# Optimization experiments

Hardware: AMD Instinct MI355X
Metric: run time of the kernel (lower is better)

The kernel has to match this reference:

```python
import jax, jax.numpy as jnp
import numpy as np

N = 50000      # nodes
E = 800000     # edges
IN = 128       # in_channels
HID = 64       # hidden_channels (per head)
HEADS = 2      # GAT heads
OUT = 64       # out_channels (classes)


def segment_softmax(e, seg, num_segments):
    # softmax of per-edge scores grouped by destination node
    m = jax.ops.segment_max(e, seg, num_segments=num_segments)
    ex = jnp.exp(e - m[seg])
    s = jax.ops.segment_sum(ex, seg, num_segments=num_segments)
    return ex / s[seg]


def setup_inputs() -> dict:
    key = jax.random.key(0)
    ks = jax.random.split(key, 12)
    sc = 0.05
    return {
        "x": jax.random.normal(ks[0], (N, IN), dtype=jnp.float32),
        "edge_index": jax.random.randint(ks[1], (2, E), 0, N),
        # GATConv params: lin (no bias), att_src/att_dst, output bias
        "W1": jax.random.normal(ks[2], (IN, HEADS * HID), dtype=jnp.float32) * sc,
        "att_src": jax.random.normal(ks[3], (HEADS, HID), dtype=jnp.float32) * sc,
        "att_dst": jax.random.normal(ks[4], (HEADS, HID), dtype=jnp.float32) * sc,
        "b1": jnp.zeros((HEADS * HID,), dtype=jnp.float32),
        # TransformerConv params (heads=1): q/k/v linears + skip linear
        "Wq": jax.random.normal(ks[5], (HEADS * HID, OUT), dtype=jnp.float32) * sc,
        "bq": jnp.zeros((OUT,), dtype=jnp.float32),
        "Wk": jax.random.normal(ks[6], (HEADS * HID, OUT), dtype=jnp.float32) * sc,
        "bk": jnp.zeros((OUT,), dtype=jnp.float32),
        "Wv": jax.random.normal(ks[7], (HEADS * HID, OUT), dtype=jnp.float32) * sc,
        "bv": jnp.zeros((OUT,), dtype=jnp.float32),
        "Wskip": jax.random.normal(ks[8], (HEADS * HID, OUT), dtype=jnp.float32) * sc,
        "bskip": jnp.zeros((OUT,), dtype=jnp.float32),
    }


def reference(x, edge_index, W1, att_src, att_dst, b1,
              Wq, bq, Wk, bk, Wv, bv, Wskip, bskip):
    n = x.shape[0]
    # ---- GATConv (concat=True, add_self_loops=True, negative_slope=0.2) ----
    loops = jnp.arange(n)
    src = jnp.concatenate([edge_index[0], loops])  # message source j
    dst = jnp.concatenate([edge_index[1], loops])  # message target i
    h = (x @ W1).reshape(n, HEADS, HID)            # [N,H,C]
    a_src = (h * att_src).sum(-1)                  # [N,H]
    a_dst = (h * att_dst).sum(-1)                  # [N,H]
    e = jax.nn.leaky_relu(a_src[src] + a_dst[dst], 0.2)   # [E+N,H]
    alpha = segment_softmax(e, dst, n)                     # [E+N,H]
    out1 = jax.ops.segment_sum(alpha[..., None] * h[src], dst, num_segments=n)
    x1 = jax.nn.relu(out1.reshape(n, HEADS * HID) + b1)    # [N,H*C]
    # ---- TransformerConv (heads=1, root_weight=True, no self-loops) ----
    q = x1 @ Wq + bq
    k = x1 @ Wk + bk
    v = x1 @ Wv + bv
    s2, d2 = edge_index[0], edge_index[1]
    scores = (q[d2] * k[s2]).sum(-1) / jnp.sqrt(jnp.float32(OUT))  # [E]
    al = segment_softmax(scores, d2, n)
    agg = jax.ops.segment_sum(al[:, None] * v[s2], d2, num_segments=n)
    out = agg + x1 @ Wskip + bskip
    return jax.nn.log_softmax(out, axis=1)
```

## Files before the change

### kernel.cpp

```cpp
#include <hip/hip_runtime.h>
#include <math.h>

typedef unsigned short u16;
typedef unsigned int u32;
typedef unsigned char u8;

using bf16x8 = __attribute__((ext_vector_type(8))) short;
using f32x4  = __attribute__((ext_vector_type(4))) float;
typedef __attribute__((ext_vector_type(2))) float vf2;

__device__ __forceinline__ float lrelu02(float x){ return x > 0.f ? x : 0.2f * x; }

__device__ __forceinline__ float bf2f(u16 u){
  union { u32 i; float f; } v; v.i = ((u32)u) << 16; return v.f;
}
__device__ __forceinline__ u16 f2bf(float f){
  union { float ff; u32 i; } v; v.ff = f;
  u32 x = v.i;
  return (u16)((x + 0x7fffu + ((x >> 16) & 1u)) >> 16);
}
__device__ __forceinline__ u32 pack2(float lo, float hi){
  return (u32)f2bf(lo) | ((u32)f2bf(hi) << 16);
}
__device__ __forceinline__ u8 f2fp8(float v){
  return (u8)(__builtin_amdgcn_cvt_pk_fp8_f32(v, v, 0, false) & 0xff);
}
__device__ __forceinline__ vf2 fma2(vf2 a, vf2 b, vf2 c){
  return __builtin_elementwise_fma(a, b, c);
}

__global__ __launch_bounds__(256) void prep_w_kernel(const float* __restrict__ W1,
                                                     const float* __restrict__ Wq,
                                                     const float* __restrict__ Wk,
                                                     const float* __restrict__ Wv,
                                                     const float* __restrict__ Ws,
                                                     const float* __restrict__ att_src,
                                                     const float* __restrict__ att_dst,
                                                     u16* __restrict__ w1t,
                                                     u16* __restrict__ wt2,
                                                     u16* __restrict__ wxt){
  int idx = blockIdx.x * 256 + threadIdx.x;
  if (idx < 16384){
    int j = idx >> 7, k = idx & 127;
    w1t[j * 128 + k] = f2bf(W1[k * 128 + j]);
  } else if (idx < 49152){
    int i = idx - 16384;
    int mat = i >> 13;
    int r = i & 8191;
    int j = r >> 7, k = r & 127;
    const float* W = (mat == 0) ? Wq : (mat == 1) ? Wk : (mat == 2) ? Wv : Ws;
    wt2[(mat * 64 + j) * 128 + k] = f2bf(W[k * 64 + j]);
  } else if (idx < 49664){
    int i = idx - 49152;
    int j = i >> 7, k = i & 127;
    const float* av = (j & 2) ? att_dst : att_src;
    int head = j & 1;
    float s = 0.f;
#pragma unroll 8
    for (int c = 0; c < 64; c++) s += W1[k * 128 + head * 64 + c] * av[head * 64 + c];
    wxt[j * 128 + k] = f2bf(s);
  } else if (idx < 51200){
    int i = idx - 49664;
    wxt[512 + i] = 0;
  }
}

__global__ __launch_bounds__(256) void gemm1_mfma(const float* __restrict__ x,
                                                  const u16* __restrict__ w1t,
                                                  const u16* __restrict__ wxt,
                                                  u8* __restrict__ h8,
                                                  float* __restrict__ asrc,
                                                  float* __restrict__ adst, int n){
  __shared__ u8 lds8[64 * 128];
  int wid = threadIdx.x >> 6, lane = threadIdx.x & 63;
  int rl = lane & 15, kh = lane >> 4;
  int br = blockIdx.x * 64 + wid * 16;
  int arow = br + rl; if (arow > n - 1) arow = n - 1;
  const float* ab = x + (size_t)arow * 128 + kh * 8;
  f32x4 acc[9];
#pragma unroll
  for (int t = 0; t < 9; t++) acc[t] = (f32x4){0.f, 0.f, 0.f, 0.f};
#pragma unroll
  for (int ks = 0; ks < 4; ks++){
    float4 xa = *(const float4*)(ab + ks * 32);
    float4 xb = *(const float4*)(ab + ks * 32 + 4);
    union { bf16x8 v; u32 w[4]; } au;
    au.w[0] = pack2(xa.x, xa.y);
    au.w[1] = pack2(xa.z, xa.w);
    au.w[2] = pack2(xb.x, xb.y);
    au.w[3] = pack2(xb.z, xb.w);
    bf16x8 a = au.v;
#pragma unroll
    for (int t = 0; t < 8; t++){
      bf16x8 b = *(const bf16x8*)(w1t + (size_t)(t * 16 + rl) * 128 + ks * 32 + kh * 8);
      acc[t] = __builtin_amdgcn_mfma_f32_16x16x32_bf16(a, b, acc[t], 0, 0, 0);
    }
    bf16x8 bx = *(const bf16x8*)(wxt + (size_t)rl * 128 + ks * 32 + kh * 8);
    acc[8] = __builtin_amdgcn_mfma_f32_16x16x32_bf16(a, bx, acc[8], 0, 0, 0);
  }
#pragma unroll
  for (int r = 0; r < 4; r++){
    int rloc = wid * 16 + kh * 4 + r;
#pragma unroll
    for (int t = 0; t < 8; t++)
      lds8[rloc * 128 + t * 16 + rl] = f2fp8(acc[t][r]);
    int orow = br + kh * 4 + r;
    if (orow < n && rl < 4){
      float vlv = acc[8][r];
      if (rl < 2) asrc[orow * 2 + rl] = vlv;
      else        adst[orow * 2 + (rl - 2)] = vlv;
    }
  }
  int rrow = wid * 16 + (lane >> 2);
  int cb = (lane & 3) * 32;
  int grow = blockIdx.x * 64 + rrow;
  if (grow < n){
    uint4 v0 = *(const uint4*)&lds8[rrow * 128 + cb];
    uint4 v1 = *(const uint4*)&lds8[rrow * 128 + cb + 16];
    uint4* gp = (uint4*)(h8 + (size_t)grow * 128 + cb);
    gp[0] = v0;
    gp[1] = v1;
  }
}

__global__ __launch_bounds__(256) void gemm2_mfma(const u16* __restrict__ x1bf,
                                                  const u16* __restrict__ wt2,
                                                  const float* __restrict__ bq,
                                                  const float* __restrict__ bk,
                                                  const float* __restrict__ bv,
                                                  const float* __restrict__ bs,
                                                  float* __restrict__ q,
                                                  u8* __restrict__ kv8,
                                                  float* __restrict__ skip, int n){
  int wid = threadIdx.x >> 6, lane = threadIdx.x & 63;
  int rl = lane & 15, kh = lane >> 4;
  int br = blockIdx.x * 64 + wid * 16;
  int arow = br + rl; if (arow > n - 1) arow = n - 1;
  const u16* abase = x1bf + (size_t)arow * 128 + kh * 8;
  f32x4 acc[16];
#pragma unroll
  for (int t = 0; t < 16; t++) acc[t] = (f32x4){0.f, 0.f, 0.f, 0.f};
#pragma unroll
  for (int ks = 0; ks < 4; ks++){
    bf16x8 a = *(const bf16x8*)(abase + ks * 32);
#pragma unroll
    for (int t = 0; t < 16; t++){
      bf16x8 b = *(const bf16x8*)(wt2 + (size_t)(t * 16 + rl) * 128 + ks * 32 + kh * 8);
      acc[t] = __builtin_amdgcn_mfma_f32_16x16x32_bf16(a, b, acc[t], 0, 0, 0);
    }
  }
  float bias_t[16];
#pragma unroll
  for (int t = 0; t < 16; t++){
    const float* bb = (t < 4) ? bq : (t < 8) ? bk : (t < 12) ? bv : bs;
    bias_t[t] = bb[(t & 3) * 16 + rl];
  }
  int orow0 = br + kh * 4;
#pragma unroll
  for (int r = 0; r < 4; r++){
    int orow = orow0 + r;
    if (orow >= n) continue;
#pragma unroll
    for (int t = 0; t < 16; t++){
      int c = (t & 3) * 16 + rl;
      float val = acc[t][r] + bias_t[t];
      if (t < 4)       q[(size_t)orow * 64 + c]    = val;
      else if (t < 8)  kv8[(size_t)orow * 128 + (c >> 3) * 16 + (c & 7)]     = f2fp8(val);
      else if (t < 12) kv8[(size_t)orow * 128 + (c >> 3) * 16 + 8 + (c & 7)] = f2fp8(val);
      else             skip[(size_t)orow * 64 + c] = val;
    }
  }
}

__global__ __launch_bounds__(256) void bucket_hist_kernel(const int* __restrict__ dst,
                                                          int* __restrict__ bc, int E){
  __shared__ int h[512];
  for (int i = threadIdx.x; i < 512; i += 256) h[i] = 0;
  __syncthreads();
  int base = blockIdx.x * 4096;
#pragma unroll
  for (int i = 0; i < 16; i++){
    int e = base + i * 256 + threadIdx.x;
    if (e < E) atomicAdd(&h[dst[e] >> 7], 1);
  }
  __syncthreads();
  for (int i = threadIdx.x; i < 512; i += 256)
    if (h[i]) atomicAdd(&bc[i], h[i]);
}

__global__ __launch_bounds__(256) void bucket_scan_kernel(const int* __restrict__ bc,
                                                          int* __restrict__ bbase,
                                                          int* __restrict__ bcur){
  __shared__ int tmp[5];
  int tid = threadIdx.x;
  int c0 = bc[2 * tid], c1 = bc[2 * tid + 1];
  int s = c0 + c1, incl = s;
  int lane = tid & 63, wid = tid >> 6;
#pragma unroll
  for (int o = 1; o < 64; o <<= 1){
    int t = __shfl_up(incl, o);
    if (lane >= o) incl += t;
  }
  if (lane == 63) tmp[wid] = incl;
  __syncthreads();
  if (tid == 0){
    int run = 0;
#pragma unroll
    for (int w2 = 0; w2 < 4; w2++){ int t = tmp[w2]; tmp[w2] = run; run += t; }
    tmp[4] = run;
  }
  __syncthreads();
  int excl = tmp[wid] + incl - s;
  bbase[2 * tid]     = excl;      bbase[2 * tid + 1] = excl + c0;
  bcur[2 * tid]      = excl;      bcur[2 * tid + 1]  = excl + c0;
  if (tid == 255) bbase[512] = tmp[4];
}

__global__ __launch_bounds__(256) void multisplit_kernel(const int* __restrict__ src,
                                                         const int* __restrict__ dst,
                                                         int* __restrict__ bcur,
                                                         uint2* __restrict__ ebuf, int E){
  __shared__ int h[512];
  __shared__ int gb[512];
  __shared__ int cur[512];
  int tid = threadIdx.x;
  for (int i = tid; i < 512; i += 256){ h[i] = 0; cur[i] = 0; }
  __syncthreads();
  int base = blockIdx.x * 4096;
  int myd[16];
#pragma unroll
  for (int i = 0; i < 16; i++){
    int e = base + i * 256 + tid;
    myd[i] = (e < E) ? dst[e] : -1;
    if (myd[i] >= 0) atomicAdd(&h[myd[i] >> 7], 1);
  }
  __syncthreads();
  for (int i = tid; i < 512; i += 256){
    int c = h[i];
    gb[i] = c ? atomicAdd(&bcur[i], c) : 0;
  }
  __syncthreads();
#pragma unroll
  for (int i = 0; i < 16; i++){
    if (myd[i] >= 0){
      int e = base + i * 256 + tid;
      int b = myd[i] >> 7;
      int r = atomicAdd(&cur[b], 1);
      uint2 ed; ed.x = (u32)src[e]; ed.y = (u32)myd[i];
      ebuf[gb[b] + r] = ed;
    }
  }
}

__global__ __launch_bounds__(256) void bucket_csr_kernel(const uint2* __restrict__ ebuf,
                                                         const int* __restrict__ bbase,
                                                         const float* __restrict__ asrc,
                                                         const float* __restrict__ adst,
                                                         int* __restrict__ offsets,
                                                         int* __restrict__ csr,
                                                         float2* __restrict__ pe,
                                                         int n, int E, int nb){
  __shared__ int deg[128];
  __shared__ int loff[128];
  __shared__ int cur[128];
  int b = blockIdx.x, tid = threadIdx.x;
  int base = bbase[b], end = bbase[b + 1];
  if (tid < 128) deg[tid] = 0;
  __syncthreads();
  for (int e = base + tid; e < end; e += 256)
    atomicAdd(&deg[ebuf[e].y & 127], 1);
  __syncthreads();
  if (tid < 64){
    int v0 = deg[2 * tid], v1 = deg[2 * tid + 1];
    int s = v0 + v1, incl = s;
#pragma unroll
    for (int o = 1; o < 64; o <<= 1){
      int t = __shfl_up(incl, o);
      if (tid >= o) incl += t;
    }
    int excl = incl - s;
    loff[2 * tid] = excl; loff[2 * tid + 1] = excl + v0;
  }
  __syncthreads();
  int node0 = b << 7;
  if (tid < 128){
    cur[tid] = loff[tid];
    int node = node0 + tid;
    if (node < n) offsets[node] = base + loff[tid];
  }
  if (b == nb - 1 && tid == 0) offsets[n] = E;
  __syncthreads();
  for (int e = base + tid; e < end; e += 256){
    uint2 ed = ebuf[e];
    int li = (int)(ed.y & 127);
    int r = atomicAdd(&cur[li], 1);
    int sj = (int)ed.x;
    csr[base + r] = sj;
    float2 as = ((const float2*)asrc)[sj];
    float2 ad = ((const float2*)adst)[node0 + li];
    float2 pv;
    pv.x = __expf(lrelu02(as.x + ad.x));
    pv.y = __expf(lrelu02(as.y + ad.y));
    pe[base + r] = pv;
  }
}

__global__ __launch_bounds__(256) void gat_agg_kernel(const u8* __restrict__ h8,
                                                      const float* __restrict__ asrc,
                                                      const float* __restrict__ adst,
                                                      const int* __restrict__ off,
                                                      const int* __restrict__ csr_src,
                                                      const float2* __restrict__ pe,
                                                      const float* __restrict__ b1,
                                                      u16* __restrict__ x1bf, int n){
  int node = blockIdx.x * 4 + (threadIdx.x >> 6);
  int lane = threadIdx.x & 63;
  if (node >= n) return;
  int s0 = off[node];
  int d  = off[node + 1] - s0;
  int g = lane >> 3;
  int sub = lane & 7;
  int chb = sub * 16;
  int head = sub >> 2;
  float2 ad  = ((const float2*)adst)[node];
  float2 asl = ((const float2*)asrc)[node];
  float ad_own = head ? ad.y : ad.x;
  float pself = __expf(lrelu02((head ? asl.y : asl.x) + ad_own));
  vf2 acc[8];
#pragma unroll
  for (int i = 0; i < 8; i++) acc[i] = (vf2){0.f, 0.f};
  float ps = 0.f;
#pragma unroll 2
  for (int base = 0; base < d; base += 8){
    int idx = base + g;
    bool valid = idx < d;
    int ee = s0 + (valid ? idx : d - 1);
    int sj = csr_src[ee];
    float2 pv = pe[ee];
    float p = valid ? (head ? pv.y : pv.x) : 0.f;
    ps += p;
    uint4 w = *(const uint4*)(h8 + (size_t)sj * 128 + chb);
    vf2 p2 = {p, p};
    acc[0] = fma2(p2, __builtin_amdgcn_cvt_pk_f32_fp8((int)w.x, false), acc[0]);
    acc[1] = fma2(p2, __builtin_amdgcn_cvt_pk_f32_fp8((int)w.x, true),  acc[1]);
    acc[2] = fma2(p2, __builtin_amdgcn_cvt_pk_f32_fp8((int)w.y, false), acc[2]);
    acc[3] = fma2(p2, __builtin_amdgcn_cvt_pk_f32_fp8((int)w.y, true),  acc[3]);
    acc[4] = fma2(p2, __builtin_amdgcn_cvt_pk_f32_fp8((int)w.z, false), acc[4]);
    acc[5] = fma2(p2, __builtin_amdgcn_cvt_pk_f32_fp8((int)w.z, true),  acc[5]);
    acc[6] = fma2(p2, __builtin_amdgcn_cvt_pk_f32_fp8((int)w.w, false), acc[6]);
    acc[7] = fma2(p2, __builtin_amdgcn_cvt_pk_f32_fp8((int)w.w, true),  acc[7]);
  }
#pragma unroll
  for (int o = 8; o <= 32; o <<= 1){
#pragma unroll
    for (int i = 0; i < 8; i++){
      acc[i][0] += __shfl_xor(acc[i][0], o);
      acc[i][1] += __shfl_xor(acc[i][1], o);
    }
    ps += __shfl_xor(ps, o);
  }
  if (lane < 8){
    ps *= 0.125f;
    ps *= 8.f;
    float st = ps + pself;
    uint4 w = *(const uint4*)(h8 + (size_t)node * 128 + chb);
    vf2 pf2 = {pself, pself};
    acc[0] = fma2(pf2, __builtin_amdgcn_cvt_pk_f32_fp8((int)w.x, false), acc[0]);
    acc[1] = fma2(pf2, __builtin_amdgcn_cvt_pk_f32_fp8((int)w.x, true),  acc[1]);
    acc[2] = fma2(pf2, __builtin_amdgcn_cvt_pk_f32_fp8((int)w.y, false), acc[2]);
    acc[3] = fma2(pf2, __builtin_amdgcn_cvt_pk_f32_fp8((int)w.y, true),  acc[3]);
    acc[4] = fma2(pf2, __builtin_amdgcn_cvt_pk_f32_fp8((int)w.z, false), acc[4]);
    acc[5] = fma2(pf2, __builtin_amdgcn_cvt_pk_f32_fp8((int)w.z, true),  acc[5]);
    acc[6] = fma2(pf2, __builtin_amdgcn_cvt_pk_f32_fp8((int)w.w, false), acc[6]);
    acc[7] = fma2(pf2, __builtin_amdgcn_cvt_pk_f32_fp8((int)w.w, true),  acc[7]);
    const float4* bp = (const float4*)(b1 + chb);
    float4 bv0 = bp[0], bv1 = bp[1], bv2 = bp[2], bv3 = bp[3];
    float bb[16] = {bv0.x, bv0.y, bv0.z, bv0.w, bv1.x, bv1.y, bv1.z, bv1.w,
                    bv2.x, bv2.y, bv2.z, bv2.w, bv3.x, bv3.y, bv3.z, bv3.w};
    float inv = 1.f / st;
    u32 wv[8];
#pragma unroll
    for (int i = 0; i < 8; i++){
      float v0 = fmaxf(acc[i][0] * inv + bb[2*i],   0.f);
      float v1 = fmaxf(acc[i][1] * inv + bb[2*i+1], 0.f);
      wv[i] = pack2(v0, v1);
    }
    uint4 o0 = {wv[0], wv[1], wv[2], wv[3]};
    uint4 o1 = {wv[4], wv[5], wv[6], wv[7]};
    u16* xp = x1bf + (size_t)node * 128 + chb;
    *(uint4*)xp = o0;
    *(uint4*)(xp + 8) = o1;
  }
}

__global__ __launch_bounds__(256) void trans_agg_kernel(const float* __restrict__ q,
                                                        const u8* __restrict__ kv8,
                                                        const float* __restrict__ skip,
                                                        const int* __restrict__ off,
                                                        const int* __restrict__ csr_src,
                                                        float* __restrict__ out, int n){
  int node = blockIdx.x * 4 + (threadIdx.x >> 6);
  int lane = threadIdx.x & 63;
  if (node >= n) return;
  int s0 = off[node];
  int d  = off[node + 1] - s0;
  int g = lane >> 3;
  int sub = lane & 7;
  const vf2* qp = (const vf2*)(q + (size_t)node * 64 + sub * 8);
  vf2 q0 = qp[0], q1 = qp[1], q2 = qp[2], q3 = qp[3];
  vf2 acc[4];
#pragma unroll
  for (int i = 0; i < 4; i++) acc[i] = (vf2){0.f, 0.f};
  float ps = 0.f;
#pragma unroll 2
  for (int base = 0; base < d; base += 8){
    int idx = base + g;
    bool valid = idx < d;
    int sj = csr_src[s0 + (valid ? idx : d - 1)];
    uint4 w = *(const uint4*)(kv8 + (size_t)sj * 128 + sub * 16);
    vf2 d2 = {0.f, 0.f};
    d2 = fma2(q0, __builtin_amdgcn_cvt_pk_f32_fp8((int)w.x, false), d2);
    d2 = fma2(q1, __builtin_amdgcn_cvt_pk_f32_fp8((int)w.x, true),  d2);
    d2 = fma2(q2, __builtin_amdgcn_cvt_pk_f32_fp8((int)w.y, false), d2);
    d2 = fma2(q3, __builtin_amdgcn_cvt_pk_f32_fp8((int)w.y, true),  d2);
    float part = d2[0] + d2[1];
    part += __shfl_xor(part, 1);
    part += __shfl_xor(part, 2);
    part += __shfl_xor(part, 4);
    float p = valid ? __expf(part * 0.125f) : 0.f;
    ps += p;
    vf2 p2 = {p, p};
    acc[0] = fma2(p2, __builtin_amdgcn_cvt_pk_f32_fp8((int)w.z, false), acc[0]);
    acc[1] = fma2(p2, __builtin_amdgcn_cvt_pk_f32_fp8((int)w.z, true),  acc[1]);
    acc[2] = fma2(p2, __builtin_amdgcn_cvt_pk_f32_fp8((int)w.w, false), acc[2]);
    acc[3] = fma2(p2, __builtin_amdgcn_cvt_pk_f32_fp8((int)w.w, true),  acc[3]);
  }
#pragma unroll
  for (int o = 8; o <= 32; o <<= 1){
#pragma unroll
    for (int i = 0; i < 4; i++){
      acc[i][0] += __shfl_xor(acc[i][0], o);
      acc[i][1] += __shfl_xor(acc[i][1], o);
    }
    ps += __shfl_xor(ps, o);
  }
  if (lane < 8){
    const float4* sp = (const float4*)(skip + (size_t)node * 64 + sub * 8);
    float4 s0v = sp[0], s1v = sp[1];
    float sk[8] = {s0v.x, s0v.y, s0v.z, s0v.w, s1v.x, s1v.y, s1v.z, s1v.w};
    float inv = (d > 0) ? 1.f / ps : 0.f;
    float val[8];
    float mx = -3.0e38f;
#pragma unroll
    for (int i = 0; i < 8; i++){
      val[i] = sk[i] + acc[i >> 1][i & 1] * inv;
      mx = fmaxf(mx, val[i]);
    }
    mx = fmaxf(mx, __shfl_xor(mx, 1));
    mx = fmaxf(mx, __shfl_xor(mx, 2));
    mx = fmaxf(mx, __shfl_xor(mx, 4));
    float se = 0.f;
#pragma unroll
    for (int i = 0; i < 8; i++){ val[i] -= mx; se += __expf(val[i]); }
    se += __shfl_xor(se, 1);
    se += __shfl_xor(se, 2);
    se += __shfl_xor(se, 4);
    float lse = __logf(se);
    float* op = out + (size_t)node * 64 + sub * 8;
    float4 o0 = {val[0] - lse, val[1] - lse, val[2] - lse, val[3] - lse};
    float4 o4 = {val[4] - lse, val[5] - lse, val[6] - lse, val[7] - lse};
    *(float4*)(op)     = o0;
    *(float4*)(op + 4) = o4;
  }
}

extern "C" void kernel_launch(void* const* d_in, const int* in_sizes, int n_in,
                              void* d_out, int out_size, void* d_ws, size_t ws_size,
                              hipStream_t stream) {
  const float* x       = (const float*)d_in[0];
  const int*   ei      = (const int*)d_in[1];
  const float* W1      = (const float*)d_in[2];
  const float* att_src = (const float*)d_in[3];
  const float* att_dst = (const float*)d_in[4];
  const float* b1      = (const float*)d_in[5];
  const float* Wq = (const float*)d_in[6];  const float* bq = (const float*)d_in[7];
  const float* Wk = (const float*)d_in[8];  const float* bk = (const float*)d_in[9];
  const float* Wv = (const float*)d_in[10]; const float* bv = (const float*)d_in[11];
  const float* Ws = (const float*)d_in[12]; const float* bs = (const float*)d_in[13];
  float* out = (float*)d_out;

  int n = in_sizes[0] / 128;
  int E = in_sizes[1] / 2;
  const int* src = ei;
  const int* dst = ei + E;
  int nb = (n + 127) >> 7;

  char* w = (char*)d_ws;
  auto alloc = [&](size_t bytes) -> void* {
    void* p = (void*)w;
    w += (bytes + 255) & ~(size_t)255;
    return p;
  };
  u8*   h8   = (u8*)alloc((size_t)n * 128);
  float* asrc = (float*)alloc((size_t)n * 2 * 4);
  float* adst = (float*)alloc((size_t)n * 2 * 4);
  u16*  x1bf = (u16*)alloc((size_t)n * 128 * 2);
  float* qq   = (float*)alloc((size_t)n * 64 * 4);
  u8*   kv8  = (u8*)alloc((size_t)n * 128);
  float* skip = (float*)alloc((size_t)n * 64 * 4);
  int* offsets = (int*)alloc((size_t)(n + 1) * 4);
  int* csr     = (int*)alloc((size_t)E * 4);
  float2* pe   = (float2*)alloc((size_t)E * 8);
  int* bc      = (int*)alloc(516 * 4);
  int* bbase   = (int*)alloc(516 * 4);
  int* bcur    = (int*)alloc(516 * 4);
  u16*  w1t  = (u16*)alloc((size_t)128 * 128 * 2);
  u16*  wt2  = (u16*)alloc((size_t)256 * 128 * 2);
  u16*  wxt  = (u16*)alloc((size_t)16 * 128 * 2);
  uint2* ebuf = (uint2*)x1bf;

  int eblocks = (E + 4095) / 4096;

  hipMemsetAsync(bc, 0, 513 * 4, stream);
  prep_w_kernel<<<200, 256, 0, stream>>>(W1, Wq, Wk, Wv, Ws, att_src, att_dst,
                                         w1t, wt2, wxt);
  gemm1_mfma<<<(n + 63) / 64, 256, 0, stream>>>(x, w1t, wxt, h8, asrc, adst, n);

  bucket_hist_kernel<<<eblocks, 256, 0, stream>>>(dst, bc, E);
  bucket_scan_kernel<<<1, 256, 0, stream>>>(bc, bbase, bcur);
  multisplit_kernel<<<eblocks, 256, 0, stream>>>(src, dst, bcur, ebuf, E);
  bucket_csr_kernel<<<nb, 256, 0, stream>>>(ebuf, bbase, asrc, adst,
                                            offsets, csr, pe, n, E, nb);

  gat_agg_kernel<<<(n + 3) / 4, 256, 0, stream>>>(h8, asrc, adst, offsets, csr, pe,
                                                  b1, x1bf, n);

  gemm2_mfma<<<(n + 63) / 64, 256, 0, stream>>>(x1bf, wt2, bq, bk, bv, bs,
                                                qq, kv8, skip, n);
  trans_agg_kernel<<<(n + 3) / 4, 256, 0, stream>>>(qq, kv8, skip, offsets, csr,
                                                    out, n);
}
```

Measured before the change: 180.0 us.

## Fuse GAT aggregation with second projection GEMM and compress edge weights to bf16

Merges the GAT aggregation kernel with the q/k/v/skip projection GEMM. Each block aggregates four nodes into LDS as bf16, then each wave runs MFMA for one of the four output matrices, so the x1 intermediate never goes to global memory. Per-edge softmax numerators are stored as packed bf16 pairs instead of float2, halving that buffer, and the bucket-count memset is folded into the weight-prep kernel. The cost is that each 4-node block rereads the full 64KB weight matrix, only 4 of 16 MFMA rows carry useful data, and edge weights lose precision.

```diff
diff --git a/kernel.cpp b/kernel.cpp
--- a/kernel.cpp
+++ b/kernel.cpp
@@ -38,7 +38,8 @@
                                                      const float* __restrict__ att_dst,
                                                      u16* __restrict__ w1t,
                                                      u16* __restrict__ wt2,
-                                                     u16* __restrict__ wxt){
+                                                     u16* __restrict__ wxt,
+                                                     int* __restrict__ bc){
   int idx = blockIdx.x * 256 + threadIdx.x;
   if (idx < 16384){
     int j = idx >> 7, k = idx & 127;
@@ -62,6 +63,8 @@
   } else if (idx < 51200){
     int i = idx - 49664;
     wxt[512 + i] = 0;
+  } else if (idx < 51713){
+    bc[idx - 51200] = 0;
   }
 }
 
@@ -123,55 +126,6 @@
   }
 }
 
-__global__ __launch_bounds__(256) void gemm2_mfma(const u16* __restrict__ x1bf,
-                                                  const u16* __restrict__ wt2,
-                                                  const float* __restrict__ bq,
-                                                  const float* __restrict__ bk,
-                                                  const float* __restrict__ bv,
-                                                  const float* __restrict__ bs,
-                                                  float* __restrict__ q,
-                                                  u8* __restrict__ kv8,
-                                                  float* __restrict__ skip, int n){
-  int wid = threadIdx.x >> 6, lane = threadIdx.x & 63;
-  int rl = lane & 15, kh = lane >> 4;
-  int br = blockIdx.x * 64 + wid * 16;
-  int arow = br + rl; if (arow > n - 1) arow = n - 1;
-  const u16* abase = x1bf + (size_t)arow * 128 + kh * 8;
-  f32x4 acc[16];
-#pragma unroll
-  for (int t = 0; t < 16; t++) acc[t] = (f32x4){0.f, 0.f, 0.f, 0.f};
-#pragma unroll
-  for (int ks = 0; ks < 4; ks++){
-    bf16x8 a = *(const bf16x8*)(abase + ks * 32);
-#pragma unroll
-    for (int t = 0; t < 16; t++){
-      bf16x8 b = *(const bf16x8*)(wt2 + (size_t)(t * 16 + rl) * 128 + ks * 32 + kh * 8);
-      acc[t] = __builtin_amdgcn_mfma_f32_16x16x32_bf16(a, b, acc[t], 0, 0, 0);
-    }
-  }
-  float bias_t[16];
-#pragma unroll
-  for (int t = 0; t < 16; t++){
-    const float* bb = (t < 4) ? bq : (t < 8) ? bk : (t < 12) ? bv : bs;
-    bias_t[t] = bb[(t & 3) * 16 + rl];
-  }
-  int orow0 = br + kh * 4;
-#pragma unroll
-  for (int r = 0; r < 4; r++){
-    int orow = orow0 + r;
-    if (orow >= n) continue;
-#pragma unroll
-    for (int t = 0; t < 16; t++){
-      int c = (t & 3) * 16 + rl;
-      float val = acc[t][r] + bias_t[t];
-      if (t < 4)       q[(size_t)orow * 64 + c]    = val;
-      else if (t < 8)  kv8[(size_t)orow * 128 + (c >> 3) * 16 + (c & 7)]     = f2fp8(val);
-      else if (t < 12) kv8[(size_t)orow * 128 + (c >> 3) * 16 + 8 + (c & 7)] = f2fp8(val);
-      else             skip[(size_t)orow * 64 + c] = val;
-    }
-  }
-}
-
 __global__ __launch_bounds__(256) void bucket_hist_kernel(const int* __restrict__ dst,
                                                           int* __restrict__ bc, int E){
   __shared__ int h[512];
@@ -258,7 +212,7 @@
                                                          const float* __restrict__ adst,
                                                          int* __restrict__ offsets,
                                                          int* __restrict__ csr,
-                                                         float2* __restrict__ pe,
+                                                         u32* __restrict__ pe,
                                                          int n, int E, int nb){
   __shared__ int deg[128];
   __shared__ int loff[128];
@@ -298,98 +252,134 @@
     csr[base + r] = sj;
     float2 as = ((const float2*)asrc)[sj];
     float2 ad = ((const float2*)adst)[node0 + li];
-    float2 pv;
-    pv.x = __expf(lrelu02(as.x + ad.x));
-    pv.y = __expf(lrelu02(as.y + ad.y));
-    pe[base + r] = pv;
-  }
-}
-
-__global__ __launch_bounds__(256) void gat_agg_kernel(const u8* __restrict__ h8,
-                                                      const float* __restrict__ asrc,
-                                                      const float* __restrict__ adst,
-                                                      const int* __restrict__ off,
-                                                      const int* __restrict__ csr_src,
-                                                      const float2* __restrict__ pe,
-                                                      const float* __restrict__ b1,
-                                                      u16* __restrict__ x1bf, int n){
-  int node = blockIdx.x * 4 + (threadIdx.x >> 6);
-  int lane = threadIdx.x & 63;
-  if (node >= n) return;
-  int s0 = off[node];
-  int d  = off[node + 1] - s0;
-  int g = lane >> 3;
-  int sub = lane & 7;
-  int chb = sub * 16;
-  int head = sub >> 2;
-  float2 ad  = ((const float2*)adst)[node];
-  float2 asl = ((const float2*)asrc)[node];
-  float ad_own = head ? ad.y : ad.x;
-  float pself = __expf(lrelu02((head ? asl.y : asl.x) + ad_own));
-  vf2 acc[8];
-#pragma unroll
-  for (int i = 0; i < 8; i++) acc[i] = (vf2){0.f, 0.f};
-  float ps = 0.f;
+    pe[base + r] = pack2(__expf(lrelu02(as.x + ad.x)),
+                         __expf(lrelu02(as.y + ad.y)));
+  }
+}
+
+__global__ __launch_bounds__(256) void gat_gemm2_kernel(const u8* __restrict__ h8,
+                                                        const float* __restrict__ asrc,
+                                                        const float* __restrict__ adst,
+                                                        const int* __restrict__ off,
+                                                        const int* __restrict__ csr_src,
+                                                        const u32* __restrict__ pe,
+                                                        const float* __restrict__ b1,
+                                                        const u16* __restrict__ wt2,
+                                                        const float* __restrict__ bq,
+                                                        const float* __restrict__ bk,
+                                                        const float* __restrict__ bv,
+                                                        const float* __restrict__ bs,
+                                                        float* __restrict__ q,
+                                                        u8* __restrict__ kv8,
+                                                        float* __restrict__ skip, int n){
+  __shared__ u16 xs[4][128];
+  int wid = threadIdx.x >> 6, lane = threadIdx.x & 63;
+  int node = blockIdx.x * 4 + wid;
+  if (node < n){
+    int s0 = off[node];
+    int d  = off[node + 1] - s0;
+    int g = lane >> 3;
+    int sub = lane & 7;
+    int chb = sub * 16;
+    int head = sub >> 2;
+    float2 ad  = ((const float2*)adst)[node];
+    float2 asl = ((const float2*)asrc)[node];
+    float ad_own = head ? ad.y : ad.x;
+    float pself = __expf(lrelu02((head ? asl.y : asl.x) + ad_own));
+    vf2 acc[8];
+#pragma unroll
+    for (int i = 0; i < 8; i++) acc[i] = (vf2){0.f, 0.f};
+    float ps = 0.f;
 #pragma unroll 2
-  for (int base = 0; base < d; base += 8){
-    int idx = base + g;
-    bool valid = idx < d;
-    int ee = s0 + (valid ? idx : d - 1);
-    int sj = csr_src[ee];
-    float2 pv = pe[ee];
-    float p = valid ? (head ? pv.y : pv.x) : 0.f;
-    ps += p;
-    uint4 w = *(const uint4*)(h8 + (size_t)sj * 128 + chb);
-    vf2 p2 = {p, p};
-    acc[0] = fma2(p2, __builtin_amdgcn_cvt_pk_f32_fp8((int)w.x, false), acc[0]);
-    acc[1] = fma2(p2, __builtin_amdgcn_cvt_pk_f32_fp8((int)w.x, true),  acc[1]);
-    acc[2] = fma2(p2, __builtin_amdgcn_cvt_pk_f32_fp8((int)w.y, false), acc[2]);
-    acc[3] = fma2(p2, __builtin_amdgcn_cvt_pk_f32_fp8((int)w.y, true),  acc[3]);
-    acc[4] = fma2(p2, __builtin_amdgcn_cvt_pk_f32_fp8((int)w.z, false), acc[4]);
-    acc[5] = fma2(p2, __builtin_amdgcn_cvt_pk_f32_fp8((int)w.z, true),  acc[5]);
-    acc[6] = fma2(p2, __builtin_amdgcn_cvt_pk_f32_fp8((int)w.w, false), acc[6]);
-    acc[7] = fma2(p2, __builtin_amdgcn_cvt_pk_f32_fp8((int)w.w, true),  acc[7]);
-  }
-#pragma unroll
-  for (int o = 8; o <= 32; o <<= 1){
-#pragma unroll
-    for (int i = 0; i < 8; i++){
-      acc[i][0] += __shfl_xor(acc[i][0], o);
-      acc[i][1] += __shfl_xor(acc[i][1], o);
-    }
-    ps += __shfl_xor(ps, o);
-  }
-  if (lane < 8){
-    ps *= 0.125f;
-    ps *= 8.f;
-    float st = ps + pself;
-    uint4 w = *(const uint4*)(h8 + (size_t)node * 128 + chb);
-    vf2 pf2 = {pself, pself};
-    acc[0] = fma2(pf2, __builtin_amdgcn_cvt_pk_f32_fp8((int)w.x, false), acc[0]);
-    acc[1] = fma2(pf2, __builtin_amdgcn_cvt_pk_f32_fp8((int)w.x, true),  acc[1]);
-    acc[2] = fma2(pf2, __builtin_amdgcn_cvt_pk_f32_fp8((int)w.y, false), acc[2]);
-    acc[3] = fma2(pf2, __builtin_amdgcn_cvt_pk_f32_fp8((int)w.y, true),  acc[3]);
-    acc[4] = fma2(pf2, __builtin_amdgcn_cvt_pk_f32_fp8((int)w.z, false), acc[4]);
-    acc[5] = fma2(pf2, __builtin_amdgcn_cvt_pk_f32_fp8((int)w.z, true),  acc[5]);
-    acc[6] = fma2(pf2, __builtin_amdgcn_cvt_pk_f32_fp8((int)w.w, false), acc[6]);
-    acc[7] = fma2(pf2, __builtin_amdgcn_cvt_pk_f32_fp8((int)w.w, true),  acc[7]);
-    const float4* bp = (const float4*)(b1 + chb);
-    float4 bv0 = bp[0], bv1 = bp[1], bv2 = bp[2], bv3 = bp[3];
-    float bb[16] = {bv0.x, bv0.y, bv0.z, bv0.w, bv1.x, bv1.y, bv1.z, bv1.w,
-                    bv2.x, bv2.y, bv2.z, bv2.w, bv3.x, bv3.y, bv3.z, bv3.w};
-    float inv = 1.f / st;
-    u32 wv[8];
-#pragma unroll
-    for (int i = 0; i < 8; i++){
-      float v0 = fmaxf(acc[i][0] * inv + bb[2*i],   0.f);
-      float v1 = fmaxf(acc[i][1] * inv + bb[2*i+1], 0.f);
-      wv[i] = pack2(v0, v1);
-    }
-    uint4 o0 = {wv[0], wv[1], wv[2], wv[3]};
-    uint4 o1 = {wv[4], wv[5], wv[6], wv[7]};
-    u16* xp = x1bf + (size_t)node * 128 + chb;
-    *(uint4*)xp = o0;
-    *(uint4*)(xp + 8) = o1;
+    for (int base = 0; base < d; base += 8){
+      int idx = base + g;
+      bool valid = idx < d;
+      int ee = s0 + (valid ? idx : d - 1);
+      int sj = csr_src[ee];
+      u32 pp = pe[ee];
+      float p = valid ? bf2f((u16)(head ? (pp >> 16) : (pp & 0xffffu))) : 0.f;
+      ps += p;
+      uint4 w = *(const uint4*)(h8 + (size_t)sj * 128 + chb);
+      vf2 p2 = {p, p};
+      acc[0] = fma2(p2, __builtin_amdgcn_cvt_pk_f32_fp8((int)w.x, false), acc[0]);
+      acc[1] = fma2(p2, __builtin_amdgcn_cvt_pk_f32_fp8((int)w.x, true),  acc[1]);
+      acc[2] = fma2(p2, __builtin_amdgcn_cvt_pk_f32_fp8((int)w.y, false), acc[2]);
+      acc[3] = fma2(p2, __builtin_amdgcn_cvt_pk_f32_fp8((int)w.y, true),  acc[3]);
+      acc[4] = fma2(p2, __builtin_amdgcn_cvt_pk_f32_fp8((int)w.z, false), acc[4]);
+      acc[5] = fma2(p2, __builtin_amdgcn_cvt_pk_f32_fp8((int)w.z, true),  acc[5]);
+      acc[6] = fma2(p2, __builtin_amdgcn_cvt_pk_f32_fp8((int)w.w, false), acc[6]);
+      acc[7] = fma2(p2, __builtin_amdgcn_cvt_pk_f32_fp8((int)w.w, true),  acc[7]);
+    }
+#pragma unroll
+    for (int o = 8; o <= 32; o <<= 1){
+#pragma unroll
+      for (int i = 0; i < 8; i++){
+        acc[i][0] += __shfl_xor(acc[i][0], o);
+        acc[i][1] += __shfl_xor(acc[i][1], o);
+      }
+      ps += __shfl_xor(ps, o);
+    }
+    if (lane < 8){
+      float st = ps + pself;
+      uint4 w = *(const uint4*)(h8 + (size_t)node * 128 + chb);
+      vf2 pf2 = {pself, pself};
+      acc[0] = fma2(pf2, __builtin_amdgcn_cvt_pk_f32_fp8((int)w.x, false), acc[0]);
+      acc[1] = fma2(pf2, __builtin_amdgcn_cvt_pk_f32_fp8((int)w.x, true),  acc[1]);
+      acc[2] = fma2(pf2, __builtin_amdgcn_cvt_pk_f32_fp8((int)w.y, false), acc[2]);
+      acc[3] = fma2(pf2, __builtin_amdgcn_cvt_pk_f32_fp8((int)w.y, true),  acc[3]);
+      acc[4] = fma2(pf2, __builtin_amdgcn_cvt_pk_f32_fp8((int)w.z, false), acc[4]);
+      acc[5] = fma2(pf2, __builtin_amdgcn_cvt_pk_f32_fp8((int)w.z, true),  acc[5]);
+      acc[6] = fma2(pf2, __builtin_amdgcn_cvt_pk_f32_fp8((int)w.w, false), acc[6]);
+      acc[7] = fma2(pf2, __builtin_amdgcn_cvt_pk_f32_fp8((int)w.w, true),  acc[7]);
+      const float4* bp = (const float4*)(b1 + chb);
+      float4 bv0 = bp[0], bv1 = bp[1], bv2 = bp[2], bv3 = bp[3];
+      float bb[16] = {bv0.x, bv0.y, bv0.z, bv0.w, bv1.x, bv1.y, bv1.z, bv1.w,
+                      bv2.x, bv2.y, bv2.z, bv2.w, bv3.x, bv3.y, bv3.z, bv3.w};
+      float inv = 1.f / st;
+      u32 wv[8];
+#pragma unroll
+      for (int i = 0; i < 8; i++){
+        float v0 = fmaxf(acc[i][0] * inv + bb[2*i],   0.f);
+        float v1 = fmaxf(acc[i][1] * inv + bb[2*i+1], 0.f);
+        wv[i] = pack2(v0, v1);
+      }
+      uint4 o0 = {wv[0], wv[1], wv[2], wv[3]};
+      uint4 o1 = {wv[4], wv[5], wv[6], wv[7]};
+      *(uint4*)&xs[wid][chb]     = o0;
+      *(uint4*)&xs[wid][chb + 8] = o1;
+    }
+  }
+  __syncthreads();
+  int rl = lane & 15, kh = lane >> 4;
+  f32x4 acc2[4];
+#pragma unroll
+  for (int t = 0; t < 4; t++) acc2[t] = (f32x4){0.f, 0.f, 0.f, 0.f};
+#pragma unroll
+  for (int ks = 0; ks < 4; ks++){
+    bf16x8 a = (bf16x8){0,0,0,0,0,0,0,0};
+    if (rl < 4) a = *(const bf16x8*)&xs[rl][ks * 32 + kh * 8];
+#pragma unroll
+    for (int t = 0; t < 4; t++){
+      bf16x8 b = *(const bf16x8*)(wt2 + (size_t)(wid * 64 + t * 16 + rl) * 128 + ks * 32 + kh * 8);
+      acc2[t] = __builtin_amdgcn_mfma_f32_16x16x32_bf16(a, b, acc2[t], 0, 0, 0);
+    }
+  }
+  if (kh == 0){
+    const float* bb = (wid == 0) ? bq : (wid == 1) ? bk : (wid == 2) ? bv : bs;
+#pragma unroll
+    for (int r = 0; r < 4; r++){
+      int orow = blockIdx.x * 4 + r;
+      if (orow >= n) continue;
+#pragma unroll
+      for (int t = 0; t < 4; t++){
+        int c = t * 16 + rl;
+        float val = acc2[t][r] + bb[c];
+        if (wid == 0)      q[(size_t)orow * 64 + c]    = val;
+        else if (wid == 1) kv8[(size_t)orow * 128 + (c >> 3) * 16 + (c & 7)]     = f2fp8(val);
+        else if (wid == 2) kv8[(size_t)orow * 128 + (c >> 3) * 16 + 8 + (c & 7)] = f2fp8(val);
+        else               skip[(size_t)orow * 64 + c] = val;
+      }
+    }
   }
 }
 
@@ -504,26 +494,24 @@
   u8*   h8   = (u8*)alloc((size_t)n * 128);
   float* asrc = (float*)alloc((size_t)n * 2 * 4);
   float* adst = (float*)alloc((size_t)n * 2 * 4);
-  u16*  x1bf = (u16*)alloc((size_t)n * 128 * 2);
   float* qq   = (float*)alloc((size_t)n * 64 * 4);
   u8*   kv8  = (u8*)alloc((size_t)n * 128);
   float* skip = (float*)alloc((size_t)n * 64 * 4);
   int* offsets = (int*)alloc((size_t)(n + 1) * 4);
   int* csr     = (int*)alloc((size_t)E * 4);
-  float2* pe   = (float2*)alloc((size_t)E * 8);
+  u32* pe      = (u32*)alloc((size_t)E * 4);
+  uint2* ebuf  = (uint2*)alloc((size_t)E * 8);
   int* bc      = (int*)alloc(516 * 4);
   int* bbase   = (int*)alloc(516 * 4);
   int* bcur    = (int*)alloc(516 * 4);
   u16*  w1t  = (u16*)alloc((size_t)128 * 128 * 2);
   u16*  wt2  = (u16*)alloc((size_t)256 * 128 * 2);
   u16*  wxt  = (u16*)alloc((size_t)16 * 128 * 2);
-  uint2* ebuf = (uint2*)x1bf;
 
   int eblocks = (E + 4095) / 4096;
 
-  hipMemsetAsync(bc, 0, 513 * 4, stream);
-  prep_w_kernel<<<200, 256, 0, stream>>>(W1, Wq, Wk, Wv, Ws, att_src, att_dst,
-                                         w1t, wt2, wxt);
+  prep_w_kernel<<<203, 256, 0, stream>>>(W1, Wq, Wk, Wv, Ws, att_src, att_dst,
+                                         w1t, wt2, wxt, bc);
   gemm1_mfma<<<(n + 63) / 64, 256, 0, stream>>>(x, w1t, wxt, h8, asrc, adst, n);
 
   bucket_hist_kernel<<<eblocks, 256, 0, stream>>>(dst, bc, E);
@@ -532,11 +520,10 @@
   bucket_csr_kernel<<<nb, 256, 0, stream>>>(ebuf, bbase, asrc, adst,
                                             offsets, csr, pe, n, E, nb);
 
-  gat_agg_kernel<<<(n + 3) / 4, 256, 0, stream>>>(h8, asrc, adst, offsets, csr, pe,
-                                                  b1, x1bf, n);
-
-  gemm2_mfma<<<(n + 63) / 64, 256, 0, stream>>>(x1bf, wt2, bq, bk, bv, bs,
-                                                qq, kv8, skip, n);
+  gat_gemm2_kernel<<<(n + 3) / 4, 256, 0, stream>>>(h8, asrc, adst, offsets, csr, pe,
+                                                    b1, wt2, bq, bk, bv, bs,
+                                                    qq, kv8, skip, n);
+
   trans_agg_kernel<<<(n + 3) / 4, 256, 0, stream>>>(qq, kv8, skip, offsets, csr,
                                                     out, n);
 }
```

New measurement: 253.8 us. 41.0% more time.
